# Optimization experiments

Hardware: AMD Instinct MI355X
Metric: run time of the kernel (lower is better)

The kernel has to match this reference:

```python
import jax, jax.numpy as jnp
import numpy as np

B, T, S, K = 512, 16, 64, 32  # batch, delta_t, num_sensors, num_clusters


def setup_inputs() -> dict:
    key = jax.random.key(0)
    k1, k2, k3 = jax.random.split(key, 3)
    X = jax.random.normal(k1, (B, T, S), dtype=jnp.float32)
    mu = jax.random.normal(k2, (K, S), dtype=jnp.float32)            # cluster means
    A = jax.random.normal(k3, (T, K, S, S), dtype=jnp.float32)       # Toeplitz block generators
    return {"X": X, "mu": mu, "A": A}


def _build_mat(A):
    # A: [T, K, S, S] -> block-Toeplitz mat: [K, T*S, T*S]
    # block(i, j) = A[i-j].T if i >= j else A[j-i]
    T_, K_, S_, _ = A.shape
    idx = jnp.arange(T_)
    diff = idx[:, None] - idx[None, :]                 # [T, T]
    blocks = A[jnp.abs(diff)]                          # [T, T, K, S, S]
    blocks_t = jnp.swapaxes(blocks, -1, -2)
    blocks = jnp.where((diff >= 0)[:, :, None, None, None], blocks_t, blocks)
    # [T, T, K, S, S] -> [K, T, S, T, S] -> [K, T*S, T*S]
    return jnp.transpose(blocks, (2, 0, 3, 1, 4)).reshape(K_, T_ * S_, T_ * S_)


def reference(X, mu, A):
    T_, K_, S_, _ = A.shape
    # dX: [B, K, T, S] -> flatten time*sensor -> [B, K, D]
    dX = (X[:, None, :, :] - mu[None, :, None, :]).reshape(X.shape[0], K_, T_ * S_)
    mat = _build_mat(A)                                # [K, D, D]
    P1 = jnp.einsum('bkd,kde,bke->bk', dX, mat, dX)    # quadratic form
    P2 = jnp.linalg.slogdet(mat)[1]                    # [K] log|det|
    lle = -0.5 * P1 + P2[None, :]
    return jax.nn.softmax(lle, axis=-1)
```

## Files before the change

kernel.cpp:

```cpp
#include <hip/hip_runtime.h>
#include <math.h>

static constexpr int B_ = 512;
static constexpr int T_ = 16;
static constexpr int S_ = 64;
static constexpr int K_ = 32;
static constexpr int N_ = 1024;

__global__ void initk(int* __restrict__ rowmap, float* __restrict__ logdet) {
  int idx = blockIdx.x * 256 + threadIdx.x;
  if (idx < K_ * N_) rowmap[idx] = idx & (N_ - 1);
  if (idx < K_) logdet[idx] = 0.f;
}

__global__ __launch_bounds__(256) void buildM(const float* __restrict__ A, float* __restrict__ M) {
  size_t idx = (size_t)blockIdx.x * 256 + threadIdx.x;
  int k   = (int)(idx >> 18);
  int rem = (int)(idx & 262143);
  int row = rem >> 8;
  int c4  = (rem & 255) << 2;
  int i = row >> 6, a = row & 63;
  int j = c4 >> 6,  b0 = c4 & 63;
  float4 v;
  if (i >= j) {
    const float* Ad = A + ((size_t)((i - j) * K_ + k) << 12);
    v.x = Ad[(b0 + 0) * 64 + a];
    v.y = Ad[(b0 + 1) * 64 + a];
    v.z = Ad[(b0 + 2) * 64 + a];
    v.w = Ad[(b0 + 3) * 64 + a];
  } else {
    const float* Ad = A + ((size_t)((j - i) * K_ + k) << 12) + a * 64 + b0;
    v = *(const float4*)Ad;
  }
  *(float4*)(M + (idx << 2)) = v;
}

__global__ __launch_bounds__(256) void prepk(const float* __restrict__ A, const float* __restrict__ mu,
                                             float* __restrict__ rbuf, float* __restrict__ cterm) {
  int k = blockIdx.x;
  __shared__ float smu[64];
  __shared__ float sp[1024], sq[1024];
  int tid = threadIdx.x;
  if (tid < 64) smu[tid] = mu[k * 64 + tid];
  __syncthreads();
  for (int idx = tid; idx < 1024; idx += 256) {
    int d = idx >> 6, s = idx & 63;
    const float* Ad = A + ((size_t)(d * K_ + k) << 12);
    float ap = 0.f, aq = 0.f;
    for (int s2 = 0; s2 < 64; ++s2) {
      ap += Ad[s * 64 + s2] * smu[s2];
      aq += Ad[s2 * 64 + s] * smu[s2];
    }
    sp[idx] = ap; sq[idx] = aq;
  }
  __syncthreads();
  for (int idx = tid; idx < 1024; idx += 256) {
    int j = idx >> 6, s = idx & 63;
    float acc = 0.5f * (sp[s] + sq[s]);
    for (int d = 1; d < 16; ++d) {
      if (d <= 15 - j) acc += sp[d * 64 + s];
      if (d <= j)      acc += sq[d * 64 + s];
    }
    rbuf[k * 1024 + idx] = acc;
  }
  if (tid < 64) {
    float a = 16.f * sp[tid];
    for (int d = 1; d < 16; ++d) a += 2.f * (float)(16 - d) * sp[d * 64 + tid];
    a *= smu[tid];
    for (int off = 32; off; off >>= 1) a += __shfl_xor(a, off);
    if (tid == 0) cterm[k] = a;
  }
}

__global__ __launch_bounds__(256) void qkern(const float* __restrict__ X, const float* __restrict__ A,
                                             float* __restrict__ Qp) {
  int g = blockIdx.x;
  int btile = blockIdx.y;
  __shared__ float Xs[4][1024];
  __shared__ float Cs[4][4096];
  int tid = threadIdx.x;
  int wave = tid >> 6, lane = tid & 63;
  for (int t = tid; t < 4096; t += 256) {
    int bb = t >> 10, e = t & 1023;
    Xs[bb][e] = X[(size_t)(btile * 4 + bb) * 1024 + e];
  }
  float regQ[4][8];
#pragma unroll
  for (int bb = 0; bb < 4; ++bb)
#pragma unroll
    for (int kk = 0; kk < 8; ++kk) regQ[bb][kk] = 0.f;

  int a0 = (tid >> 4) << 2;
  int v0 = (tid & 15) << 2;
  for (int dd = 0; dd < 4; ++dd) {
    int d = g + (dd << 2);
    __syncthreads();
    for (int bb = 0; bb < 4; ++bb) {
      float4 r0 = {0,0,0,0}, r1 = {0,0,0,0}, r2 = {0,0,0,0}, r3 = {0,0,0,0};
      for (int j = 0; j + d < 16; ++j) {
        const float4 xa = *(const float4*)&Xs[bb][j * 64 + a0];
        const float4 xv = *(const float4*)&Xs[bb][(j + d) * 64 + v0];
        r0.x += xa.x * xv.x; r0.y += xa.x * xv.y; r0.z += xa.x * xv.z; r0.w += xa.x * xv.w;
        r1.x += xa.y * xv.x; r1.y += xa.y * xv.y; r1.z += xa.y * xv.z; r1.w += xa.y * xv.w;
        r2.x += xa.z * xv.x; r2.y += xa.z * xv.y; r2.z += xa.z * xv.z; r2.w += xa.z * xv.w;
        r3.x += xa.w * xv.x; r3.y += xa.w * xv.y; r3.z += xa.w * xv.z; r3.w += xa.w * xv.w;
      }
      *(float4*)&Cs[bb][(a0 + 0) * 64 + v0] = r0;
      *(float4*)&Cs[bb][(a0 + 1) * 64 + v0] = r1;
      *(float4*)&Cs[bb][(a0 + 2) * 64 + v0] = r2;
      *(float4*)&Cs[bb][(a0 + 3) * 64 + v0] = r3;
    }
    __syncthreads();
    float w = (d == 0) ? 1.f : 2.f;
    for (int ch = 0; ch < 16; ++ch) {
      int e4 = (ch * 64 + lane) << 2;
      float4 cv[4];
#pragma unroll
      for (int bb = 0; bb < 4; ++bb) {
        float4 t4 = *(const float4*)&Cs[bb][e4];
        cv[bb].x = w * t4.x; cv[bb].y = w * t4.y; cv[bb].z = w * t4.z; cv[bb].w = w * t4.w;
      }
#pragma unroll
      for (int kk = 0; kk < 8; ++kk) {
        int k = wave + (kk << 2);
        const float4 av = *(const float4*)(A + (((size_t)(d * K_ + k)) << 12) + e4);
#pragma unroll
        for (int bb = 0; bb < 4; ++bb)
          regQ[bb][kk] += av.x * cv[bb].x + av.y * cv[bb].y + av.z * cv[bb].z + av.w * cv[bb].w;
      }
    }
  }
#pragma unroll
  for (int bb = 0; bb < 4; ++bb)
#pragma unroll
    for (int kk = 0; kk < 8; ++kk) {
      float v = regQ[bb][kk];
      for (int off = 32; off; off >>= 1) v += __shfl_xor(v, off);
      regQ[bb][kk] = v;
    }
  if (lane == 0) {
    int b = btile * 4;
#pragma unroll
    for (int bb = 0; bb < 4; ++bb)
#pragma unroll
      for (int kk = 0; kk < 8; ++kk)
        Qp[((size_t)(g * B_ + b + bb) << 5) + (wave + (kk << 2))] = regQ[bb][kk];
  }
}

__global__ __launch_bounds__(1024) void panelk(float* __restrict__ M, int* __restrict__ rowmap,
                                               float* __restrict__ logdet, int j0) {
  int k = blockIdx.x;
  float* Mk = M + ((size_t)k << 20);
  int* rmk = rowmap + (k << 10);
  int m = N_ - j0;
  int t = threadIdx.x;
  int bdim = blockDim.x;
  int lane = t & 63, wid = t >> 6;
  int nw = (bdim + 63) >> 6;

  __shared__ float bufP[32];
  __shared__ float bufJ[32];
  __shared__ int origP, origJ;
  __shared__ float candv[16];
  __shared__ int candi[16];
  __shared__ int spiv;

  float r[32];
  int myorig = -1;
  float mydiag = 1.f;
  bool act = (t < m);
  if (act) {
    myorig = rmk[j0 + t];
    const float* src = Mk + (size_t)myorig * N_ + j0;
#pragma unroll
    for (int c4 = 0; c4 < 8; ++c4) *(float4*)&r[c4 * 4] = *(const float4*)(src + c4 * 4);
  }

#pragma unroll
  for (int jj = 0; jj < 32; ++jj) {
    float bv = (act && t >= jj) ? fabsf(r[jj]) : -1.f;
    int bi = t;
#pragma unroll
    for (int off = 32; off; off >>= 1) {
      float ov = __shfl_xor(bv, off);
      int oi = __shfl_xor(bi, off);
      if (ov > bv) { bv = ov; bi = oi; }
    }
    if (lane == 0) { candv[wid] = bv; candi[wid] = bi; }
    __syncthreads();
    if (t < 64) {
      float cv = (lane < nw) ? candv[lane] : -1.f;
      int ci = (lane < nw) ? candi[lane] : 0;
#pragma unroll
      for (int off = 8; off; off >>= 1) {
        float ov = __shfl_down(cv, off, 16);
        int oi = __shfl_down(ci, off, 16);
        if (ov > cv) { cv = ov; ci = oi; }
      }
      if (lane == 0) spiv = ci;
    }
    __syncthreads();
    int p = spiv;
    if (t == p) {
#pragma unroll
      for (int c4 = 0; c4 < 8; ++c4) *(float4*)&bufP[c4 * 4] = *(const float4*)&r[c4 * 4];
      origP = myorig;
    }
    if (p != jj && t == jj) {
#pragma unroll
      for (int c4 = 0; c4 < 8; ++c4) *(float4*)&bufJ[c4 * 4] = *(const float4*)&r[c4 * 4];
      origJ = myorig;
    }
    __syncthreads();
    float pr[32];
#pragma unroll
    for (int c4 = 0; c4 < 8; ++c4) *(float4*)&pr[c4 * 4] = *(const float4*)&bufP[c4 * 4];
    if (p != jj) {
      if (t == jj) {
#pragma unroll
        for (int c = 0; c < 32; ++c) r[c] = pr[c];
        myorig = origP;
      } else if (t == p) {
#pragma unroll
        for (int c4 = 0; c4 < 8; ++c4) *(float4*)&r[c4 * 4] = *(const float4*)&bufJ[c4 * 4];
        myorig = origJ;
      }
    }
    float pv = pr[jj];
    if (t == jj) mydiag = pv;
    float sinv = 1.0f / pv;
    if (act && t > jj) {
      float mult = r[jj] * sinv;
      r[jj] = mult;
#pragma unroll
      for (int c = jj + 1; c < 32; ++c) r[c] -= mult * pr[c];
    }
  }

  if (t < 32) {
    float lv = logf(fabsf(mydiag));
#pragma unroll
    for (int off = 16; off; off >>= 1) lv += __shfl_down(lv, off, 32);
    if (t == 0) logdet[k] += lv;
  }
  if (act) {
    float* dst = Mk + (size_t)(j0 + t) * N_ + j0;
#pragma unroll
    for (int c4 = 0; c4 < 8; ++c4) *(float4*)(dst + c4 * 4) = *(const float4*)&r[c4 * 4];
    rmk[j0 + t] = myorig;
  }
}

__global__ __launch_bounds__(256) void updatek(float* __restrict__ M, const int* __restrict__ rowmap, int j0) {
  int k = blockIdx.z;
  int mprime = N_ - j0 - 32;
  int r0 = blockIdx.y << 7;
  int c0 = blockIdx.x << 7;
  float* Mk = M + ((size_t)k << 20);
  const int* rmk = rowmap + (k << 10);
  __shared__ float l11[32 * 36];
  __shared__ float LtT[32 * 132];
  __shared__ float Ut[32 * 132];
  __shared__ int rowL[128];
  __shared__ int prU[32];
  int tid = threadIdx.x;

  if (tid < 128) rowL[tid] = (r0 + tid < mprime) ? rmk[j0 + 32 + r0 + tid] : -1;
  else if (tid < 160) prU[tid - 128] = rmk[j0 + (tid - 128)];
  {
    int rr = tid >> 3, q = (tid & 7) << 2;
    *(float4*)&l11[rr * 36 + q] = *(const float4*)(Mk + (size_t)(j0 + rr) * N_ + j0 + q);
  }
  for (int x = tid; x < 1024; x += 256) {
    int i = x >> 3, q = (x & 7) << 2;
    float4 v = {0.f, 0.f, 0.f, 0.f};
    if (r0 + i < mprime) v = *(const float4*)(Mk + (size_t)(j0 + 32 + r0 + i) * N_ + j0 + q);
    LtT[(q + 0) * 132 + i] = v.x;
    LtT[(q + 1) * 132 + i] = v.y;
    LtT[(q + 2) * 132 + i] = v.z;
    LtT[(q + 3) * 132 + i] = v.w;
  }
  __syncthreads();

  if (tid < 128) {
    int c = c0 + tid;
    bool ok = (c < mprime);
    float u[32];
#pragma unroll
    for (int rr = 0; rr < 32; ++rr) {
      float av = ok ? Mk[(size_t)prU[rr] * N_ + j0 + 32 + c] : 0.f;
#pragma unroll
      for (int t = 0; t < rr; ++t) av -= l11[rr * 36 + t] * u[t];
      u[rr] = av;
      Ut[rr * 132 + tid] = av;
    }
  }
  __syncthreads();

  int tx = tid & 15, ty = tid >> 4;
  float4 acc[2][2][4];
#pragma unroll
  for (int a = 0; a < 2; ++a)
#pragma unroll
    for (int b = 0; b < 2; ++b)
#pragma unroll
      for (int r = 0; r < 4; ++r) acc[a][b][r] = make_float4(0.f, 0.f, 0.f, 0.f);

#pragma unroll 8
  for (int t = 0; t < 32; ++t) {
    float4 aL = *(const float4*)&LtT[t * 132 + (ty << 2)];
    float4 aH = *(const float4*)&LtT[t * 132 + (ty << 2) + 64];
    float4 bL = *(const float4*)&Ut[t * 132 + (tx << 2)];
    float4 bH = *(const float4*)&Ut[t * 132 + (tx << 2) + 64];
#define FMA4(dst, s, b4) dst.x += (s) * b4.x; dst.y += (s) * b4.y; dst.z += (s) * b4.z; dst.w += (s) * b4.w;
    FMA4(acc[0][0][0], aL.x, bL) FMA4(acc[0][0][1], aL.y, bL) FMA4(acc[0][0][2], aL.z, bL) FMA4(acc[0][0][3], aL.w, bL)
    FMA4(acc[0][1][0], aL.x, bH) FMA4(acc[0][1][1], aL.y, bH) FMA4(acc[0][1][2], aL.z, bH) FMA4(acc[0][1][3], aL.w, bH)
    FMA4(acc[1][0][0], aH.x, bL) FMA4(acc[1][0][1], aH.y, bL) FMA4(acc[1][0][2], aH.z, bL) FMA4(acc[1][0][3], aH.w, bL)
    FMA4(acc[1][1][0], aH.x, bH) FMA4(acc[1][1][1], aH.y, bH) FMA4(acc[1][1][2], aH.z, bH) FMA4(acc[1][1][3], aH.w, bH)
#undef FMA4
  }

#pragma unroll
  for (int ri = 0; ri < 2; ++ri)
#pragma unroll
    for (int r = 0; r < 4; ++r) {
      int lr = (ty << 2) + r + (ri << 6);
      int pr = rowL[lr];
      if (pr < 0) continue;
      float* rowp = Mk + (size_t)pr * N_ + j0 + 32 + c0;
#pragma unroll
      for (int ci = 0; ci < 2; ++ci) {
        int lc = (tx << 2) + (ci << 6);
        if (c0 + lc < mprime) {
          float4* p = (float4*)(rowp + lc);
          float4 cur = *p;
          cur.x -= acc[ri][ci][r].x;
          cur.y -= acc[ri][ci][r].y;
          cur.z -= acc[ri][ci][r].z;
          cur.w -= acc[ri][ci][r].w;
          *p = cur;
        }
      }
    }
}

__global__ __launch_bounds__(256) void finalk(const float* __restrict__ X, const float* __restrict__ rbuf,
                                              const float* __restrict__ cterm, const float* __restrict__ logdet,
                                              const float* __restrict__ Qp, float* __restrict__ out) {
  int b = blockIdx.x;
  __shared__ float Xs[1024];
  __shared__ float lleS[32];
  int tid = threadIdx.x, wave = tid >> 6, lane = tid & 63;
  for (int i = tid; i < 1024; i += 256) Xs[i] = X[(size_t)b * 1024 + i];
  __syncthreads();
#pragma unroll
  for (int kk = 0; kk < 8; ++kk) {
    int k = wave + (kk << 2);
    const float* rk = rbuf + (size_t)k * 1024;
    float acc = 0.f;
#pragma unroll
    for (int ch = 0; ch < 4; ++ch) {
      int e4 = (ch * 64 + lane) << 2;
      const float4 rv = *(const float4*)(rk + e4);
      const float4 xv = *(const float4*)&Xs[e4];
      acc += rv.x * xv.x + rv.y * xv.y + rv.z * xv.z + rv.w * xv.w;
    }
    for (int off = 32; off; off >>= 1) acc += __shfl_xor(acc, off);
    if (lane == 0) {
      float Qv = 0.f;
#pragma unroll
      for (int g = 0; g < 4; ++g) Qv += Qp[((size_t)(g * B_ + b) << 5) + k];
      float P1 = Qv - 2.f * acc + cterm[k];
      lleS[k] = -0.5f * P1 + logdet[k];
    }
  }
  __syncthreads();
  if (wave == 0) {
    float v = lleS[lane & 31];
    float mx = v;
    for (int off = 16; off; off >>= 1) mx = fmaxf(mx, __shfl_xor(mx, off));
    float e = expf(v - mx);
    float s = e;
    for (int off = 16; off; off >>= 1) s += __shfl_xor(s, off);
    if (lane < 32) out[b * 32 + lane] = e / s;
  }
}

extern "C" void kernel_launch(void* const* d_in, const int* in_sizes, int n_in,
                              void* d_out, int out_size, void* d_ws, size_t ws_size,
                              hipStream_t stream) {
  const float* X  = (const float*)d_in[0];
  const float* mu = (const float*)d_in[1];
  const float* A  = (const float*)d_in[2];
  float* out = (float*)d_out;
  float* ws  = (float*)d_ws;

  if (ws_size < 134742272ull) {
    hipMemsetAsync(d_out, 0, (size_t)out_size * sizeof(float), stream);
    return;
  }

  float* M      = ws;
  int*   rowmap = (int*)(ws + 33554432);
  float* logdet = ws + 33587200;
  float* rbuf   = ws + 33587232;
  float* cterm  = ws + 33620000;
  float* Qp     = ws + 33620032;

  initk<<<dim3(128), dim3(256), 0, stream>>>(rowmap, logdet);
  buildM<<<dim3(32768), dim3(256), 0, stream>>>(A, M);
  prepk<<<dim3(32), dim3(256), 0, stream>>>(A, mu, rbuf, cterm);
  qkern<<<dim3(4, 128), dim3(256), 0, stream>>>(X, A, Qp);

  for (int s = 0; s < 32; ++s) {
    int j0 = s * 32;
    int m = N_ - j0;
    int bt = ((m + 63) >> 6) << 6;
    panelk<<<dim3(32), dim3(bt), 0, stream>>>(M, rowmap, logdet, j0);
    int mprime = m - 32;
    if (mprime > 0) {
      int mt = (mprime + 127) >> 7;
      updatek<<<dim3(mt, mt, 32), dim3(256), 0, stream>>>(M, rowmap, j0);
    }
  }

  finalk<<<dim3(512), dim3(256), 0, stream>>>(X, rbuf, cterm, logdet, Qp, out);
}
```

Measured before the change: 3.006 ms.

## Widen LU panel to 64 columns and tile buildM by 64x64 blocks

The blocked LU factorization now uses 64-column panels, which halves the number of panel and trailing-update launches. The panel kernel keeps 64-wide rows in registers and merges the next column's pivot search into the current elimination step, saving one barrier per column. The update kernel solves the 64x64 triangular block and accumulates the trailing GEMM in two 32-wide chunks. buildM now copies each Toeplitz block as a 64x64 tile, transposing through shared memory so that reads are coalesced. In exchange, each panel thread holds more registers, and the serial panel work per step is longer.

```diff
diff --git a/kernel.cpp b/kernel.cpp
--- a/kernel.cpp
+++ b/kernel.cpp
@@ -14,25 +14,32 @@
 }
 
 __global__ __launch_bounds__(256) void buildM(const float* __restrict__ A, float* __restrict__ M) {
-  size_t idx = (size_t)blockIdx.x * 256 + threadIdx.x;
-  int k   = (int)(idx >> 18);
-  int rem = (int)(idx & 262143);
-  int row = rem >> 8;
-  int c4  = (rem & 255) << 2;
-  int i = row >> 6, a = row & 63;
-  int j = c4 >> 6,  b0 = c4 & 63;
-  float4 v;
-  if (i >= j) {
-    const float* Ad = A + ((size_t)((i - j) * K_ + k) << 12);
-    v.x = Ad[(b0 + 0) * 64 + a];
-    v.y = Ad[(b0 + 1) * 64 + a];
-    v.z = Ad[(b0 + 2) * 64 + a];
-    v.w = Ad[(b0 + 3) * 64 + a];
+  int k = blockIdx.z, i = blockIdx.y, j = blockIdx.x;
+  int d = i - j;
+  int ad = d >= 0 ? d : -d;
+  const float* Ad = A + ((size_t)(ad * K_ + k) << 12);
+  float* out = M + ((size_t)k << 20) + (size_t)(i * 64) * N_ + j * 64;
+  int tid = threadIdx.x;
+  if (d < 0) {
+    for (int x = tid; x < 1024; x += 256) {
+      int a = x >> 4, b4 = (x & 15) << 2;
+      *(float4*)(out + (size_t)a * N_ + b4) = *(const float4*)(Ad + a * 64 + b4);
+    }
   } else {
-    const float* Ad = A + ((size_t)((j - i) * K_ + k) << 12) + a * 64 + b0;
-    v = *(const float4*)Ad;
-  }
-  *(float4*)(M + (idx << 2)) = v;
+    __shared__ float ts[64][65];
+    for (int x = tid; x < 1024; x += 256) {
+      int r = x >> 4, c4 = (x & 15) << 2;
+      float4 v = *(const float4*)(Ad + r * 64 + c4);
+      ts[c4 + 0][r] = v.x; ts[c4 + 1][r] = v.y; ts[c4 + 2][r] = v.z; ts[c4 + 3][r] = v.w;
+    }
+    __syncthreads();
+    for (int x = tid; x < 1024; x += 256) {
+      int a = x >> 4, b4 = (x & 15) << 2;
+      float4 v;
+      v.x = ts[a][b4 + 0]; v.y = ts[a][b4 + 1]; v.z = ts[a][b4 + 2]; v.w = ts[a][b4 + 3];
+      *(float4*)(out + (size_t)a * N_ + b4) = v;
+    }
+  }
 }
 
 __global__ __launch_bounds__(256) void prepk(const float* __restrict__ A, const float* __restrict__ mu,
@@ -155,18 +162,16 @@
   int* rmk = rowmap + (k << 10);
   int m = N_ - j0;
   int t = threadIdx.x;
-  int bdim = blockDim.x;
   int lane = t & 63, wid = t >> 6;
-  int nw = (bdim + 63) >> 6;
-
-  __shared__ float bufP[32];
-  __shared__ float bufJ[32];
+  int nw = blockDim.x >> 6;
+
+  __shared__ float bufP[64];
+  __shared__ float bufJ[64];
   __shared__ int origP, origJ;
   __shared__ float candv[16];
   __shared__ int candi[16];
-  __shared__ int spiv;
-
-  float r[32];
+
+  float r[64];
   int myorig = -1;
   float mydiag = 1.f;
   bool act = (t < m);
@@ -174,12 +179,12 @@
     myorig = rmk[j0 + t];
     const float* src = Mk + (size_t)myorig * N_ + j0;
 #pragma unroll
-    for (int c4 = 0; c4 < 8; ++c4) *(float4*)&r[c4 * 4] = *(const float4*)(src + c4 * 4);
-  }
-
-#pragma unroll
-  for (int jj = 0; jj < 32; ++jj) {
-    float bv = (act && t >= jj) ? fabsf(r[jj]) : -1.f;
+    for (int c4 = 0; c4 < 16; ++c4) *(float4*)&r[c4 * 4] = *(const float4*)(src + c4 * 4);
+  }
+
+  int pcur;
+  {
+    float bv = act ? fabsf(r[0]) : -1.f;
     int bi = t;
 #pragma unroll
     for (int off = 32; off; off >>= 1) {
@@ -189,109 +194,131 @@
     }
     if (lane == 0) { candv[wid] = bv; candi[wid] = bi; }
     __syncthreads();
-    if (t < 64) {
-      float cv = (lane < nw) ? candv[lane] : -1.f;
-      int ci = (lane < nw) ? candi[lane] : 0;
-#pragma unroll
-      for (int off = 8; off; off >>= 1) {
-        float ov = __shfl_down(cv, off, 16);
-        int oi = __shfl_down(ci, off, 16);
-        if (ov > cv) { cv = ov; ci = oi; }
-      }
-      if (lane == 0) spiv = ci;
+    float cv = -1.f; int ci = 0;
+    for (int w = 0; w < nw; ++w) { float v = candv[w]; if (v > cv) { cv = v; ci = candi[w]; } }
+    pcur = ci;
+    if (t == pcur) {
+#pragma unroll
+      for (int c4 = 0; c4 < 16; ++c4) *(float4*)&bufP[c4 * 4] = *(const float4*)&r[c4 * 4];
+      origP = myorig;
+    }
+    if (pcur != 0 && t == 0) {
+#pragma unroll
+      for (int c4 = 0; c4 < 16; ++c4) *(float4*)&bufJ[c4 * 4] = *(const float4*)&r[c4 * 4];
+      origJ = myorig;
     }
     __syncthreads();
-    int p = spiv;
-    if (t == p) {
-#pragma unroll
-      for (int c4 = 0; c4 < 8; ++c4) *(float4*)&bufP[c4 * 4] = *(const float4*)&r[c4 * 4];
-      origP = myorig;
-    }
-    if (p != jj && t == jj) {
-#pragma unroll
-      for (int c4 = 0; c4 < 8; ++c4) *(float4*)&bufJ[c4 * 4] = *(const float4*)&r[c4 * 4];
-      origJ = myorig;
-    }
-    __syncthreads();
-    float pr[32];
-#pragma unroll
-    for (int c4 = 0; c4 < 8; ++c4) *(float4*)&pr[c4 * 4] = *(const float4*)&bufP[c4 * 4];
-    if (p != jj) {
+  }
+
+#pragma unroll
+  for (int jj = 0; jj < 64; ++jj) {
+    if (pcur != jj) {
       if (t == jj) {
 #pragma unroll
-        for (int c = 0; c < 32; ++c) r[c] = pr[c];
+        for (int c4 = 0; c4 < 16; ++c4) *(float4*)&r[c4 * 4] = *(const float4*)&bufP[c4 * 4];
         myorig = origP;
-      } else if (t == p) {
-#pragma unroll
-        for (int c4 = 0; c4 < 8; ++c4) *(float4*)&r[c4 * 4] = *(const float4*)&bufJ[c4 * 4];
+      } else if (t == pcur) {
+#pragma unroll
+        for (int c4 = 0; c4 < 16; ++c4) *(float4*)&r[c4 * 4] = *(const float4*)&bufJ[c4 * 4];
         myorig = origJ;
       }
     }
+    float pr[64];
+#pragma unroll
+    for (int c4 = jj >> 2; c4 < 16; ++c4) *(float4*)&pr[c4 * 4] = *(const float4*)&bufP[c4 * 4];
     float pv = pr[jj];
     if (t == jj) mydiag = pv;
-    float sinv = 1.0f / pv;
+    float cand = -1.f;
     if (act && t > jj) {
-      float mult = r[jj] * sinv;
+      float mult = r[jj] / pv;
       r[jj] = mult;
 #pragma unroll
-      for (int c = jj + 1; c < 32; ++c) r[c] -= mult * pr[c];
-    }
-  }
-
-  if (t < 32) {
+      for (int c = jj + 1; c < 64; ++c) r[c] -= mult * pr[c];
+      if (jj < 63) cand = fabsf(r[jj + 1]);
+    }
+    if (jj < 63) {
+      float bv = cand; int bi = t;
+#pragma unroll
+      for (int off = 32; off; off >>= 1) {
+        float ov = __shfl_xor(bv, off);
+        int oi = __shfl_xor(bi, off);
+        if (ov > bv) { bv = ov; bi = oi; }
+      }
+      if (lane == 0) { candv[wid] = bv; candi[wid] = bi; }
+      __syncthreads();
+      float cv = -1.f; int ci = jj + 1;
+      for (int w = 0; w < nw; ++w) { float v = candv[w]; if (v > cv) { cv = v; ci = candi[w]; } }
+      int pn = ci;
+      if (t == pn) {
+#pragma unroll
+        for (int c4 = 0; c4 < 16; ++c4) *(float4*)&bufP[c4 * 4] = *(const float4*)&r[c4 * 4];
+        origP = myorig;
+      }
+      if (pn != jj + 1 && t == jj + 1) {
+#pragma unroll
+        for (int c4 = 0; c4 < 16; ++c4) *(float4*)&bufJ[c4 * 4] = *(const float4*)&r[c4 * 4];
+        origJ = myorig;
+      }
+      pcur = pn;
+      __syncthreads();
+    }
+  }
+
+  if (t < 64) {
     float lv = logf(fabsf(mydiag));
 #pragma unroll
-    for (int off = 16; off; off >>= 1) lv += __shfl_down(lv, off, 32);
+    for (int off = 32; off; off >>= 1) lv += __shfl_down(lv, off);
     if (t == 0) logdet[k] += lv;
   }
   if (act) {
     float* dst = Mk + (size_t)(j0 + t) * N_ + j0;
 #pragma unroll
-    for (int c4 = 0; c4 < 8; ++c4) *(float4*)(dst + c4 * 4) = *(const float4*)&r[c4 * 4];
+    for (int c4 = 0; c4 < 16; ++c4) *(float4*)(dst + c4 * 4) = *(const float4*)&r[c4 * 4];
     rmk[j0 + t] = myorig;
   }
 }
 
 __global__ __launch_bounds__(256) void updatek(float* __restrict__ M, const int* __restrict__ rowmap, int j0) {
   int k = blockIdx.z;
-  int mprime = N_ - j0 - 32;
+  int mprime = N_ - j0 - 64;
   int r0 = blockIdx.y << 7;
   int c0 = blockIdx.x << 7;
   float* Mk = M + ((size_t)k << 20);
   const int* rmk = rowmap + (k << 10);
-  __shared__ float l11[32 * 36];
+  __shared__ float l11[64 * 68];
   __shared__ float LtT[32 * 132];
   __shared__ float Ut[32 * 132];
   __shared__ int rowL[128];
-  __shared__ int prU[32];
+  __shared__ int prU[64];
   int tid = threadIdx.x;
 
-  if (tid < 128) rowL[tid] = (r0 + tid < mprime) ? rmk[j0 + 32 + r0 + tid] : -1;
-  else if (tid < 160) prU[tid - 128] = rmk[j0 + (tid - 128)];
-  {
-    int rr = tid >> 3, q = (tid & 7) << 2;
-    *(float4*)&l11[rr * 36 + q] = *(const float4*)(Mk + (size_t)(j0 + rr) * N_ + j0 + q);
-  }
+  if (tid < 128) rowL[tid] = (r0 + tid < mprime) ? rmk[j0 + 64 + r0 + tid] : -1;
+  else if (tid < 192) prU[tid - 128] = rmk[j0 + (tid - 128)];
   for (int x = tid; x < 1024; x += 256) {
-    int i = x >> 3, q = (x & 7) << 2;
+    int rr = x >> 4, q = (x & 15) << 2;
+    *(float4*)&l11[rr * 68 + q] = *(const float4*)(Mk + (size_t)(j0 + rr) * N_ + j0 + q);
+  }
+  for (int x = tid; x < 1024; x += 256) {
+    int rI = x >> 3, q = (x & 7) << 2;
     float4 v = {0.f, 0.f, 0.f, 0.f};
-    if (r0 + i < mprime) v = *(const float4*)(Mk + (size_t)(j0 + 32 + r0 + i) * N_ + j0 + q);
-    LtT[(q + 0) * 132 + i] = v.x;
-    LtT[(q + 1) * 132 + i] = v.y;
-    LtT[(q + 2) * 132 + i] = v.z;
-    LtT[(q + 3) * 132 + i] = v.w;
-  }
-  __syncthreads();
-
-  if (tid < 128) {
-    int c = c0 + tid;
-    bool ok = (c < mprime);
-    float u[32];
+    if (r0 + rI < mprime) v = *(const float4*)(Mk + (size_t)(j0 + 64 + r0 + rI) * N_ + j0 + q);
+    LtT[(q + 0) * 132 + rI] = v.x;
+    LtT[(q + 1) * 132 + rI] = v.y;
+    LtT[(q + 2) * 132 + rI] = v.z;
+    LtT[(q + 3) * 132 + rI] = v.w;
+  }
+  __syncthreads();
+
+  float u[32];
+  bool tcol = tid < 128;
+  int c = c0 + tid;
+  bool ok = tcol && (c < mprime);
+  if (tcol) {
 #pragma unroll
     for (int rr = 0; rr < 32; ++rr) {
-      float av = ok ? Mk[(size_t)prU[rr] * N_ + j0 + 32 + c] : 0.f;
-#pragma unroll
-      for (int t = 0; t < rr; ++t) av -= l11[rr * 36 + t] * u[t];
+      float av = ok ? Mk[(size_t)prU[rr] * N_ + j0 + 64 + c] : 0.f;
+#pragma unroll
+      for (int tt = 0; tt < rr; ++tt) av -= l11[rr * 68 + tt] * u[tt];
       u[rr] = av;
       Ut[rr * 132 + tid] = av;
     }
@@ -307,20 +334,52 @@
 #pragma unroll
       for (int r = 0; r < 4; ++r) acc[a][b][r] = make_float4(0.f, 0.f, 0.f, 0.f);
 
-#pragma unroll 8
-  for (int t = 0; t < 32; ++t) {
-    float4 aL = *(const float4*)&LtT[t * 132 + (ty << 2)];
-    float4 aH = *(const float4*)&LtT[t * 132 + (ty << 2) + 64];
-    float4 bL = *(const float4*)&Ut[t * 132 + (tx << 2)];
-    float4 bH = *(const float4*)&Ut[t * 132 + (tx << 2) + 64];
 #define FMA4(dst, s, b4) dst.x += (s) * b4.x; dst.y += (s) * b4.y; dst.z += (s) * b4.z; dst.w += (s) * b4.w;
-    FMA4(acc[0][0][0], aL.x, bL) FMA4(acc[0][0][1], aL.y, bL) FMA4(acc[0][0][2], aL.z, bL) FMA4(acc[0][0][3], aL.w, bL)
-    FMA4(acc[0][1][0], aL.x, bH) FMA4(acc[0][1][1], aL.y, bH) FMA4(acc[0][1][2], aL.z, bH) FMA4(acc[0][1][3], aL.w, bH)
-    FMA4(acc[1][0][0], aH.x, bL) FMA4(acc[1][0][1], aH.y, bL) FMA4(acc[1][0][2], aH.z, bL) FMA4(acc[1][0][3], aH.w, bL)
-    FMA4(acc[1][1][0], aH.x, bH) FMA4(acc[1][1][1], aH.y, bH) FMA4(acc[1][1][2], aH.z, bH) FMA4(acc[1][1][3], aH.w, bH)
+#define GEMM_CHUNK() \
+  _Pragma("unroll 8") \
+  for (int tk = 0; tk < 32; ++tk) { \
+    float4 aL = *(const float4*)&LtT[tk * 132 + (ty << 2)]; \
+    float4 aH = *(const float4*)&LtT[tk * 132 + (ty << 2) + 64]; \
+    float4 bL = *(const float4*)&Ut[tk * 132 + (tx << 2)]; \
+    float4 bH = *(const float4*)&Ut[tk * 132 + (tx << 2) + 64]; \
+    FMA4(acc[0][0][0], aL.x, bL) FMA4(acc[0][0][1], aL.y, bL) FMA4(acc[0][0][2], aL.z, bL) FMA4(acc[0][0][3], aL.w, bL) \
+    FMA4(acc[0][1][0], aL.x, bH) FMA4(acc[0][1][1], aL.y, bH) FMA4(acc[0][1][2], aL.z, bH) FMA4(acc[0][1][3], aL.w, bH) \
+    FMA4(acc[1][0][0], aH.x, bL) FMA4(acc[1][0][1], aH.y, bL) FMA4(acc[1][0][2], aH.z, bL) FMA4(acc[1][0][3], aH.w, bL) \
+    FMA4(acc[1][1][0], aH.x, bH) FMA4(acc[1][1][1], aH.y, bH) FMA4(acc[1][1][2], aH.z, bH) FMA4(acc[1][1][3], aH.w, bH) \
+  }
+
+  GEMM_CHUNK()
+  __syncthreads();
+
+  for (int x = tid; x < 1024; x += 256) {
+    int rI = x >> 3, q = (x & 7) << 2;
+    float4 v = {0.f, 0.f, 0.f, 0.f};
+    if (r0 + rI < mprime) v = *(const float4*)(Mk + (size_t)(j0 + 64 + r0 + rI) * N_ + j0 + 32 + q);
+    LtT[(q + 0) * 132 + rI] = v.x;
+    LtT[(q + 1) * 132 + rI] = v.y;
+    LtT[(q + 2) * 132 + rI] = v.z;
+    LtT[(q + 3) * 132 + rI] = v.w;
+  }
+  if (tcol) {
+    float u2[32];
+#pragma unroll
+    for (int rr = 32; rr < 64; ++rr) {
+      float av = ok ? Mk[(size_t)prU[rr] * N_ + j0 + 64 + c] : 0.f;
+#pragma unroll
+      for (int tt = 0; tt < 32; ++tt) av -= l11[rr * 68 + tt] * u[tt];
+#pragma unroll
+      for (int tt = 32; tt < 64; ++tt) { if (tt < rr) av -= l11[rr * 68 + tt] * u2[tt - 32]; }
+      u2[rr - 32] = av;
+      Ut[(rr - 32) * 132 + tid] = av;
+    }
+  }
+  __syncthreads();
+
+  GEMM_CHUNK()
+#undef GEMM_CHUNK
 #undef FMA4
-  }
-
+
+  int cc = c0 + (tx << 2);
 #pragma unroll
   for (int ri = 0; ri < 2; ++ri)
 #pragma unroll
@@ -328,11 +387,11 @@
       int lr = (ty << 2) + r + (ri << 6);
       int pr = rowL[lr];
       if (pr < 0) continue;
-      float* rowp = Mk + (size_t)pr * N_ + j0 + 32 + c0;
+      float* rowp = Mk + (size_t)pr * N_ + j0 + 64;
 #pragma unroll
       for (int ci = 0; ci < 2; ++ci) {
-        int lc = (tx << 2) + (ci << 6);
-        if (c0 + lc < mprime) {
+        int lc = cc + (ci << 6);
+        if (lc < mprime) {
           float4* p = (float4*)(rowp + lc);
           float4 cur = *p;
           cur.x -= acc[ri][ci][r].x;
@@ -409,16 +468,15 @@
   float* Qp     = ws + 33620032;
 
   initk<<<dim3(128), dim3(256), 0, stream>>>(rowmap, logdet);
-  buildM<<<dim3(32768), dim3(256), 0, stream>>>(A, M);
+  buildM<<<dim3(16, 16, 32), dim3(256), 0, stream>>>(A, M);
   prepk<<<dim3(32), dim3(256), 0, stream>>>(A, mu, rbuf, cterm);
   qkern<<<dim3(4, 128), dim3(256), 0, stream>>>(X, A, Qp);
 
-  for (int s = 0; s < 32; ++s) {
-    int j0 = s * 32;
+  for (int s = 0; s < 16; ++s) {
+    int j0 = s * 64;
     int m = N_ - j0;
-    int bt = ((m + 63) >> 6) << 6;
-    panelk<<<dim3(32), dim3(bt), 0, stream>>>(M, rowmap, logdet, j0);
-    int mprime = m - 32;
+    panelk<<<dim3(32), dim3(m), 0, stream>>>(M, rowmap, logdet, j0);
+    int mprime = m - 64;
     if (mprime > 0) {
       int mt = (mprime + 127) >> 7;
       updatek<<<dim3(mt, mt, 32), dim3(256), 0, stream>>>(M, rowmap, j0);
```

Result: slower. 11.36 ms (+277.8%).

## Compute U12 triangular solve once in panel kernel, prefetch C tile in update

Applied to the files above, without the earlier changes.

The triangular solve producing the U12 row block moves from every update tile (each tile row block recomputed it) into the panel kernel, which computes it once per column and stores it to a new workspace buffer. The update kernel then just loads U from that buffer and preloads the trailing-matrix tile into registers before the FMA loop. buildM becomes a 64x64 block-per-CTA kernel that transposes through shared memory, replacing strided gathers. The change adds serial work and register pressure to the panel kernel, which runs only 32 blocks.

```diff
diff --git a/kernel.cpp b/kernel.cpp
--- a/kernel.cpp
+++ b/kernel.cpp
@@ -14,25 +14,32 @@
 }
 
 __global__ __launch_bounds__(256) void buildM(const float* __restrict__ A, float* __restrict__ M) {
-  size_t idx = (size_t)blockIdx.x * 256 + threadIdx.x;
-  int k   = (int)(idx >> 18);
-  int rem = (int)(idx & 262143);
-  int row = rem >> 8;
-  int c4  = (rem & 255) << 2;
-  int i = row >> 6, a = row & 63;
-  int j = c4 >> 6,  b0 = c4 & 63;
-  float4 v;
-  if (i >= j) {
-    const float* Ad = A + ((size_t)((i - j) * K_ + k) << 12);
-    v.x = Ad[(b0 + 0) * 64 + a];
-    v.y = Ad[(b0 + 1) * 64 + a];
-    v.z = Ad[(b0 + 2) * 64 + a];
-    v.w = Ad[(b0 + 3) * 64 + a];
+  int k = blockIdx.z, i = blockIdx.y, j = blockIdx.x;
+  int d = i - j;
+  int ad = d >= 0 ? d : -d;
+  const float* Ad = A + ((size_t)(ad * K_ + k) << 12);
+  float* out = M + ((size_t)k << 20) + (size_t)(i * 64) * N_ + j * 64;
+  int tid = threadIdx.x;
+  if (d < 0) {
+    for (int x = tid; x < 1024; x += 256) {
+      int a = x >> 4, b4 = (x & 15) << 2;
+      *(float4*)(out + (size_t)a * N_ + b4) = *(const float4*)(Ad + a * 64 + b4);
+    }
   } else {
-    const float* Ad = A + ((size_t)((j - i) * K_ + k) << 12) + a * 64 + b0;
-    v = *(const float4*)Ad;
-  }
-  *(float4*)(M + (idx << 2)) = v;
+    __shared__ float ts[64][65];
+    for (int x = tid; x < 1024; x += 256) {
+      int r = x >> 4, c4 = (x & 15) << 2;
+      float4 v = *(const float4*)(Ad + r * 64 + c4);
+      ts[c4 + 0][r] = v.x; ts[c4 + 1][r] = v.y; ts[c4 + 2][r] = v.z; ts[c4 + 3][r] = v.w;
+    }
+    __syncthreads();
+    for (int x = tid; x < 1024; x += 256) {
+      int a = x >> 4, b4 = (x & 15) << 2;
+      float4 v;
+      v.x = ts[a][b4 + 0]; v.y = ts[a][b4 + 1]; v.z = ts[a][b4 + 2]; v.w = ts[a][b4 + 3];
+      *(float4*)(out + (size_t)a * N_ + b4) = v;
+    }
+  }
 }
 
 __global__ __launch_bounds__(256) void prepk(const float* __restrict__ A, const float* __restrict__ mu,
@@ -149,7 +156,8 @@
 }
 
 __global__ __launch_bounds__(1024) void panelk(float* __restrict__ M, int* __restrict__ rowmap,
-                                               float* __restrict__ logdet, int j0) {
+                                               float* __restrict__ logdet, float* __restrict__ Uws,
+                                               int j0) {
   int k = blockIdx.x;
   float* Mk = M + ((size_t)k << 20);
   int* rmk = rowmap + (k << 10);
@@ -165,6 +173,8 @@
   __shared__ float candv[16];
   __shared__ int candi[16];
   __shared__ int spiv;
+  __shared__ float l11s[32 * 33];
+  __shared__ int smapU[32];
 
   float r[32];
   int myorig = -1;
@@ -244,82 +254,102 @@
     for (int off = 16; off; off >>= 1) lv += __shfl_down(lv, off, 32);
     if (t == 0) logdet[k] += lv;
   }
+  if (t < 32) {
+#pragma unroll
+    for (int c = 0; c < 32; ++c) l11s[t * 33 + c] = r[c];
+    smapU[t] = myorig;
+  }
   if (act) {
     float* dst = Mk + (size_t)(j0 + t) * N_ + j0;
 #pragma unroll
     for (int c4 = 0; c4 < 8; ++c4) *(float4*)(dst + c4 * 4) = *(const float4*)&r[c4 * 4];
     rmk[j0 + t] = myorig;
   }
-}
-
-__global__ __launch_bounds__(256) void updatek(float* __restrict__ M, const int* __restrict__ rowmap, int j0) {
+  __syncthreads();
+
+  int mprime = m - 32;
+  if (t < mprime) {
+    int col = j0 + 32 + t;
+    float* Uk = Uws + ((size_t)k << 15);
+    float u[32];
+#pragma unroll
+    for (int rr = 0; rr < 32; ++rr) {
+      float av = Mk[(size_t)smapU[rr] * N_ + col];
+#pragma unroll
+      for (int tt = 0; tt < 32; ++tt) { if (tt < rr) av -= l11s[rr * 33 + tt] * u[tt]; }
+      u[rr] = av;
+      Uk[(rr << 10) + col] = av;
+    }
+  }
+}
+
+__global__ __launch_bounds__(256) void updatek(float* __restrict__ M, const int* __restrict__ rowmap,
+                                               const float* __restrict__ Uws, int j0) {
   int k = blockIdx.z;
   int mprime = N_ - j0 - 32;
   int r0 = blockIdx.y << 7;
   int c0 = blockIdx.x << 7;
   float* Mk = M + ((size_t)k << 20);
   const int* rmk = rowmap + (k << 10);
-  __shared__ float l11[32 * 36];
   __shared__ float LtT[32 * 132];
   __shared__ float Ut[32 * 132];
   __shared__ int rowL[128];
-  __shared__ int prU[32];
   int tid = threadIdx.x;
 
   if (tid < 128) rowL[tid] = (r0 + tid < mprime) ? rmk[j0 + 32 + r0 + tid] : -1;
-  else if (tid < 160) prU[tid - 128] = rmk[j0 + (tid - 128)];
+  for (int x = tid; x < 1024; x += 256) {
+    int rI = x >> 3, q = (x & 7) << 2;
+    float4 v = {0.f, 0.f, 0.f, 0.f};
+    if (r0 + rI < mprime) v = *(const float4*)(Mk + (size_t)(j0 + 32 + r0 + rI) * N_ + j0 + q);
+    LtT[(q + 0) * 132 + rI] = v.x;
+    LtT[(q + 1) * 132 + rI] = v.y;
+    LtT[(q + 2) * 132 + rI] = v.z;
+    LtT[(q + 3) * 132 + rI] = v.w;
+  }
   {
-    int rr = tid >> 3, q = (tid & 7) << 2;
-    *(float4*)&l11[rr * 36 + q] = *(const float4*)(Mk + (size_t)(j0 + rr) * N_ + j0 + q);
-  }
-  for (int x = tid; x < 1024; x += 256) {
-    int i = x >> 3, q = (x & 7) << 2;
-    float4 v = {0.f, 0.f, 0.f, 0.f};
-    if (r0 + i < mprime) v = *(const float4*)(Mk + (size_t)(j0 + 32 + r0 + i) * N_ + j0 + q);
-    LtT[(q + 0) * 132 + i] = v.x;
-    LtT[(q + 1) * 132 + i] = v.y;
-    LtT[(q + 2) * 132 + i] = v.z;
-    LtT[(q + 3) * 132 + i] = v.w;
-  }
-  __syncthreads();
-
-  if (tid < 128) {
-    int c = c0 + tid;
-    bool ok = (c < mprime);
-    float u[32];
-#pragma unroll
-    for (int rr = 0; rr < 32; ++rr) {
-      float av = ok ? Mk[(size_t)prU[rr] * N_ + j0 + 32 + c] : 0.f;
-#pragma unroll
-      for (int t = 0; t < rr; ++t) av -= l11[rr * 36 + t] * u[t];
-      u[rr] = av;
-      Ut[rr * 132 + tid] = av;
+    const float* Uk = Uws + ((size_t)k << 15) + j0 + 32 + c0;
+    for (int x = tid; x < 1024; x += 256) {
+      int rr = x >> 5, c4 = (x & 31) << 2;
+      float4 v = {0.f, 0.f, 0.f, 0.f};
+      if (c0 + c4 < mprime) v = *(const float4*)(Uk + (rr << 10) + c4);
+      *(float4*)&Ut[rr * 132 + c4] = v;
     }
   }
   __syncthreads();
 
   int tx = tid & 15, ty = tid >> 4;
-  float4 acc[2][2][4];
-#pragma unroll
-  for (int a = 0; a < 2; ++a)
-#pragma unroll
-    for (int b = 0; b < 2; ++b)
-#pragma unroll
-      for (int r = 0; r < 4; ++r) acc[a][b][r] = make_float4(0.f, 0.f, 0.f, 0.f);
-
+  int cc = c0 + (tx << 2);
+
+  float4 cur[2][2][4];
+#pragma unroll
+  for (int ri = 0; ri < 2; ++ri)
+#pragma unroll
+    for (int r = 0; r < 4; ++r) {
+      int lr = (ty << 2) + r + (ri << 6);
+      int pr = rowL[lr];
+#pragma unroll
+      for (int ci = 0; ci < 2; ++ci) {
+        int lc = cc + (ci << 6);
+        if (pr >= 0 && lc < mprime)
+          cur[ri][ci][r] = *(const float4*)(Mk + (size_t)pr * N_ + j0 + 32 + lc);
+        else
+          cur[ri][ci][r] = make_float4(0.f, 0.f, 0.f, 0.f);
+      }
+    }
+
+#define FMS4(dst, s, b4) dst.x -= (s) * b4.x; dst.y -= (s) * b4.y; dst.z -= (s) * b4.z; dst.w -= (s) * b4.w;
 #pragma unroll 8
-  for (int t = 0; t < 32; ++t) {
-    float4 aL = *(const float4*)&LtT[t * 132 + (ty << 2)];
-    float4 aH = *(const float4*)&LtT[t * 132 + (ty << 2) + 64];
-    float4 bL = *(const float4*)&Ut[t * 132 + (tx << 2)];
-    float4 bH = *(const float4*)&Ut[t * 132 + (tx << 2) + 64];
-#define FMA4(dst, s, b4) dst.x += (s) * b4.x; dst.y += (s) * b4.y; dst.z += (s) * b4.z; dst.w += (s) * b4.w;
-    FMA4(acc[0][0][0], aL.x, bL) FMA4(acc[0][0][1], aL.y, bL) FMA4(acc[0][0][2], aL.z, bL) FMA4(acc[0][0][3], aL.w, bL)
-    FMA4(acc[0][1][0], aL.x, bH) FMA4(acc[0][1][1], aL.y, bH) FMA4(acc[0][1][2], aL.z, bH) FMA4(acc[0][1][3], aL.w, bH)
-    FMA4(acc[1][0][0], aH.x, bL) FMA4(acc[1][0][1], aH.y, bL) FMA4(acc[1][0][2], aH.z, bL) FMA4(acc[1][0][3], aH.w, bL)
-    FMA4(acc[1][1][0], aH.x, bH) FMA4(acc[1][1][1], aH.y, bH) FMA4(acc[1][1][2], aH.z, bH) FMA4(acc[1][1][3], aH.w, bH)
-#undef FMA4
-  }
+  for (int tk = 0; tk < 32; ++tk) {
+    float4 aL = *(const float4*)&LtT[tk * 132 + (ty << 2)];
+    float4 aH = *(const float4*)&LtT[tk * 132 + (ty << 2) + 64];
+    float4 bL = *(const float4*)&Ut[tk * 132 + (tx << 2)];
+    float4 bH = *(const float4*)&Ut[tk * 132 + (tx << 2) + 64];
+    FMS4(cur[0][0][0], aL.x, bL) FMS4(cur[0][0][1], aL.y, bL) FMS4(cur[0][0][2], aL.z, bL) FMS4(cur[0][0][3], aL.w, bL)
+    FMS4(cur[0][1][0], aL.x, bH) FMS4(cur[0][1][1], aL.y, bH) FMS4(cur[0][1][2], aL.z, bH) FMS4(cur[0][1][3], aL.w, bH)
+    FMS4(cur[1][0][0], aH.x, bL) FMS4(cur[1][0][1], aH.y, bL) FMS4(cur[1][0][2], aH.z, bL) FMS4(cur[1][0][3], aH.w, bL)
+    FMS4(cur[1][1][0], aH.x, bH) FMS4(cur[1][1][1], aH.y, bH) FMS4(cur[1][1][2], aH.z, bH) FMS4(cur[1][1][3], aH.w, bH)
+  }
+#undef FMS4
 
 #pragma unroll
   for (int ri = 0; ri < 2; ++ri)
@@ -328,19 +358,11 @@
       int lr = (ty << 2) + r + (ri << 6);
       int pr = rowL[lr];
       if (pr < 0) continue;
-      float* rowp = Mk + (size_t)pr * N_ + j0 + 32 + c0;
+      float* rowp = Mk + (size_t)pr * N_ + j0 + 32;
 #pragma unroll
       for (int ci = 0; ci < 2; ++ci) {
-        int lc = (tx << 2) + (ci << 6);
-        if (c0 + lc < mprime) {
-          float4* p = (float4*)(rowp + lc);
-          float4 cur = *p;
-          cur.x -= acc[ri][ci][r].x;
-          cur.y -= acc[ri][ci][r].y;
-          cur.z -= acc[ri][ci][r].z;
-          cur.w -= acc[ri][ci][r].w;
-          *p = cur;
-        }
+        int lc = cc + (ci << 6);
+        if (lc < mprime) *(float4*)(rowp + lc) = cur[ri][ci][r];
       }
     }
 }
@@ -396,7 +418,7 @@
   float* out = (float*)d_out;
   float* ws  = (float*)d_ws;
 
-  if (ws_size < 134742272ull) {
+  if (ws_size < 138936576ull) {
     hipMemsetAsync(d_out, 0, (size_t)out_size * sizeof(float), stream);
     return;
   }
@@ -407,9 +429,10 @@
   float* rbuf   = ws + 33587232;
   float* cterm  = ws + 33620000;
   float* Qp     = ws + 33620032;
+  float* Uws    = ws + 33685568;
 
   initk<<<dim3(128), dim3(256), 0, stream>>>(rowmap, logdet);
-  buildM<<<dim3(32768), dim3(256), 0, stream>>>(A, M);
+  buildM<<<dim3(16, 16, 32), dim3(256), 0, stream>>>(A, M);
   prepk<<<dim3(32), dim3(256), 0, stream>>>(A, mu, rbuf, cterm);
   qkern<<<dim3(4, 128), dim3(256), 0, stream>>>(X, A, Qp);
 
@@ -417,11 +440,11 @@
     int j0 = s * 32;
     int m = N_ - j0;
     int bt = ((m + 63) >> 6) << 6;
-    panelk<<<dim3(32), dim3(bt), 0, stream>>>(M, rowmap, logdet, j0);
+    panelk<<<dim3(32), dim3(bt), 0, stream>>>(M, rowmap, logdet, Uws, j0);
     int mprime = m - 32;
     if (mprime > 0) {
       int mt = (mprime + 127) >> 7;
-      updatek<<<dim3(mt, mt, 32), dim3(256), 0, stream>>>(M, rowmap, j0);
+      updatek<<<dim3(mt, mt, 32), dim3(256), 0, stream>>>(M, rowmap, Uws, j0);
     }
   }
 
```

Result: faster. 2.625 ms (-12.7%).
